# Optimization experiments

Hardware: AMD Instinct MI355X
Metric: run time of the kernel (lower is better)

Reference implementation:

```python
import jax, jax.numpy as jnp
import numpy as np

N = 10000      # nodes per graph
E = 160000     # random edges per graph (plus N self-loops)
IN_DIM = 4096
HID = 64       # num_hidden
H = 8          # heads
C = 5          # num_classes
SLOPE = 0.2    # LeakyReLU negative slope


def gat_conv(x, src, dst, W, al, ar, b, res_W=None):
    """DGL-style GATConv. x:(N,F) -> (N,H,D). Messages flow src->dst,
    edge softmax over in-edges of each dst node."""
    n = x.shape[0]
    h, d = al.shape
    feat = (x @ W).reshape(n, h, d)                      # (N,H,D)
    el = jnp.sum(feat * al, axis=-1)                     # (N,H)
    er = jnp.sum(feat * ar, axis=-1)                     # (N,H)
    e = jax.nn.leaky_relu(el[src] + er[dst], SLOPE)      # (E,H)
    emax = jax.ops.segment_max(e, dst, num_segments=n)   # (N,H) stable softmax
    ex = jnp.exp(e - emax[dst])
    denom = jax.ops.segment_sum(ex, dst, num_segments=n)
    alpha = ex / denom[dst]                              # (E,H)
    out = jax.ops.segment_sum(feat[src] * alpha[..., None], dst, num_segments=n)
    if res_W is not None:
        out = out + (x @ res_W).reshape(n, h, d)         # residual projection
    return out + b.reshape(h, d)


def encoder(x, src, dst, W0, al0, ar0, b0, W1, al1, ar1, b1):
    h0 = jax.nn.elu(gat_conv(x, src, dst, W0, al0, ar0, b0))   # (N,H,D)
    h0 = h0.reshape(h0.shape[0], -1)                           # flatten(1)
    return jax.nn.elu(gat_conv(h0, src, dst, W1, al1, ar1, b1))


def setup_inputs() -> dict:
    key = jax.random.key(0)
    ks = list(jax.random.split(key, 40))
    ki = iter(ks)

    def edges(k):
        k1, k2 = jax.random.split(k)
        loop = jnp.arange(N, dtype=jnp.int32)
        s = jnp.concatenate([jax.random.randint(k1, (E,), 0, N, dtype=jnp.int32), loop])
        d = jnp.concatenate([jax.random.randint(k2, (E,), 0, N, dtype=jnp.int32), loop])
        return s, d

    inp = {}
    for name in ("s0", "s1", "t"):
        s, d = edges(next(ki))
        inp[f"src_{name}"], inp[f"dst_{name}"] = s, d
    inp["features_s0"] = jax.random.normal(next(ki), (N, IN_DIM), jnp.float32)
    inp["features_s1"] = jax.random.normal(next(ki), (N, IN_DIM), jnp.float32)
    inp["features_t"]  = jax.random.normal(next(ki), (N, IN_DIM), jnp.float32)

    def lin(k, fan_in, fan_out):
        return jax.random.normal(k, (fan_in, fan_out), jnp.float32) / np.sqrt(fan_in)

    inp["W0"] = lin(next(ki), IN_DIM, H * HID)
    inp["al0"] = 0.1 * jax.random.normal(next(ki), (H, HID), jnp.float32)
    inp["ar0"] = 0.1 * jax.random.normal(next(ki), (H, HID), jnp.float32)
    inp["b0"] = jnp.zeros((H * HID,), jnp.float32)
    inp["W1"] = lin(next(ki), H * HID, H * HID)
    inp["al1"] = 0.1 * jax.random.normal(next(ki), (H, HID), jnp.float32)
    inp["ar1"] = 0.1 * jax.random.normal(next(ki), (H, HID), jnp.float32)
    inp["b1"] = jnp.zeros((H * HID,), jnp.float32)
    for k_idx in (0, 1):
        inp[f"Wc{k_idx}"] = lin(next(ki), H * HID, H * C)
        inp[f"alc{k_idx}"] = 0.1 * jax.random.normal(next(ki), (H, C), jnp.float32)
        inp[f"arc{k_idx}"] = 0.1 * jax.random.normal(next(ki), (H, C), jnp.float32)
        inp[f"bc{k_idx}"] = jnp.zeros((H * C,), jnp.float32)
        inp[f"rW{k_idx}"] = lin(next(ki), H * HID, H * C)
    inp["num_source"] = 2
    return inp


def reference(features_s0, features_s1, features_t,
              W0, al0, ar0, b0, W1, al1, ar1, b1,
              Wc0, alc0, arc0, bc0, rW0,
              Wc1, alc1, arc1, bc1, rW1,
              src_s0, dst_s0, src_s1, dst_s1, src_t, dst_t,
              num_source):
    enc_p = (W0, al0, ar0, b0, W1, al1, ar1, b1)
    cls_p = [(Wc0, alc0, arc0, bc0, rW0), (Wc1, alc1, arc1, bc1, rW1)]
    feats = [features_s0, features_s1]
    graphs = [(src_s0, dst_s0), (src_s1, dst_s1)]

    # shared-weight encoder on each source graph
    h_s = [encoder(feats[i], graphs[i][0], graphs[i][1], *enc_p)
           for i in range(num_source)]                    # each (N,H,HID)
    # per-source classifiers on their own graphs, mean over heads
    pred_s = []
    for i in range(num_source):
        Wc, alc, arc, bc, rW = cls_p[i]
        s, d = graphs[i]
        logits = gat_conv(h_s[i].reshape(N, -1), s, d, Wc, alc, arc, bc, res_W=rW)
        pred_s.append(logits.mean(axis=1))               # (N,C)
    emb_s = [h.reshape(N, -1) for h in h_s]

    # target: every source classifier applied to the target graph
    h_t = encoder(features_t, src_t, dst_t, *enc_p)
    pred_t = []
    for i in range(num_source):
        Wc, alc, arc, bc, rW = cls_p[i]
        logits = gat_conv(h_t.reshape(N, -1), src_t, dst_t, Wc, alc, arc, bc, res_W=rW)
        pred_t.append(logits.mean(axis=1))
    emb_t = h_t.reshape(N, -1)

    return (pred_s[0], pred_s[1], pred_t[0], pred_t[1], emb_s[0], emb_s[1], emb_t)
```

## Files before the change

### kernel.cpp

```cpp
#include <hip/hip_runtime.h>
#include <stdint.h>

typedef _Float16 f16;
typedef _Float16 f16x2 __attribute__((ext_vector_type(2)));
typedef _Float16 f16x8 __attribute__((ext_vector_type(8)));
typedef float f32x4 __attribute__((ext_vector_type(4)));

#define AS1 __attribute__((address_space(1)))
#define AS3 __attribute__((address_space(3)))

#define NN 10000
#define NP 10112
#define KK0 4096
#define FF 512

__global__ void k_count_b(const int* __restrict__ d0, const int* __restrict__ d1,
                          const int* __restrict__ d2, int E0, int E1, int E2,
                          int nb0, int nb1, int* __restrict__ deg){
  int b = blockIdx.x;
  const int* d; int Eg, base, lb;
  if (b < nb0){ d=d0; Eg=E0; base=0; lb=b; }
  else if (b < nb0+nb1){ d=d1; Eg=E1; base=NN; lb=b-nb0; }
  else { d=d2; Eg=E2; base=2*NN; lb=b-nb0-nb1; }
  int i = lb*256 + threadIdx.x;
  if (i < Eg) atomicAdd(&deg[base + d[i]], 1);
}

__global__ __launch_bounds__(1024) void k_scan_b(const int* __restrict__ deg_all,
    int* __restrict__ rowptr_all, int* __restrict__ cursor_all){
  int g = blockIdx.x;
  const int* deg = deg_all + g*NN;
  int* rowptr = rowptr_all + g*(NN+1);
  int* cursor = cursor_all + g*NN;
  __shared__ int ps[1024];
  int t = threadIdx.x;
  const int CH = 16;
  int i0 = t*CH;
  int sum = 0;
  for (int k=0;k<CH;k++){ int i=i0+k; if (i<NN) sum += deg[i]; }
  ps[t]=sum; __syncthreads();
  for (int off=1; off<1024; off<<=1){
    int v = (t>=off)? ps[t-off] : 0;
    __syncthreads();
    ps[t] += v;
    __syncthreads();
  }
  int run = ps[t]-sum;
  for (int k=0;k<CH;k++){
    int i=i0+k;
    if (i<=NN) rowptr[i]=run;
    if (i<NN){ cursor[i]=run; run += deg[i]; }
  }
}

__global__ void k_fill_b(const int* __restrict__ s0, const int* __restrict__ d0,
                         const int* __restrict__ s1, const int* __restrict__ d1,
                         const int* __restrict__ s2, const int* __restrict__ d2,
                         int E0, int E1, int E2, int nb0, int nb1,
                         int* __restrict__ cursor_all,
                         int* __restrict__ c0, int* __restrict__ c1, int* __restrict__ c2){
  int b = blockIdx.x;
  const int *s, *d; int Eg, lb; int* cur; int* col;
  if (b < nb0){ s=s0; d=d0; Eg=E0; lb=b; cur=cursor_all; col=c0; }
  else if (b < nb0+nb1){ s=s1; d=d1; Eg=E1; lb=b-nb0; cur=cursor_all+NN; col=c1; }
  else { s=s2; d=d2; Eg=E2; lb=b-nb0-nb1; cur=cursor_all+2*NN; col=c2; }
  int i = lb*256 + threadIdx.x;
  if (i >= Eg) return;
  int slot = atomicAdd(&cur[d[i]], 1);
  col[slot] = s[i];
}

__global__ void k_transpose_t(const float* __restrict__ W, f16* __restrict__ WT,
                              int K, int Nc){
  __shared__ float tile[32][33];
  int n0 = blockIdx.x*32, k0 = blockIdx.y*32;
  int tx = threadIdx.x, ty = threadIdx.y;
  #pragma unroll
  for (int i=0;i<32;i+=8)
    tile[ty+i][tx] = W[(long)(k0+ty+i)*Nc + n0+tx];
  __syncthreads();
  #pragma unroll
  for (int i=0;i<32;i+=8)
    WT[(long)(n0+ty+i)*K + k0+tx] = (f16)tile[tx][ty+i];
}

__global__ void k_pack_wc(const float* __restrict__ Wc, const float* __restrict__ rW,
                          f16* __restrict__ WT){
  int idx = blockIdx.x*256 + threadIdx.x;
  if (idx >= 128*512) return;
  int n = idx >> 9; int k = idx & 511;
  float v = 0.f;
  if (n < 40) v = Wc[k*40 + n];
  else if (n < 80) v = rW[k*40 + (n-40)];
  WT[idx] = (f16)v;
}

__global__ __launch_bounds__(256,3) void k_gemm0(
    const float* __restrict__ X0, const float* __restrict__ X1, const float* __restrict__ X2,
    f16* __restrict__ C0, f16* __restrict__ C1, f16* __restrict__ C2,
    const f16* __restrict__ B,
    const float* __restrict__ alp, const float* __restrict__ arp,
    float* __restrict__ elp, float* __restrict__ erp)
{
  __shared__ f16 lds[2][12288];
  const int bid = blockIdx.x;
  const int task = bid / 632;
  const int orig = bid - task*632;
  const int wid = (orig & 7)*79 + (orig >> 3);
  const int tr = wid >> 2, tc = wid & 3;
  const float* A = task==0 ? X0 : (task==1 ? X1 : X2);
  f16* C = task==0 ? C0 : (task==1 ? C1 : C2);

  const int t = threadIdx.x;
  const int wave = t >> 6, lane = t & 63;
  const int wr = wave >> 1, wc = wave & 1;

  const f16* Bb = B + (long)tc*128*KK0;
  const int slot = (lane&7) ^ (lane>>3);
  const int rbase = wave*8 + (lane>>3);

  const int arow0 = t >> 3;
  const int ak8 = t & 7;
  const float* gA[2];
  bool okA[2];
  #pragma unroll
  for (int s=0;s<2;s++){
    int grow = tr*64 + arow0 + s*32;
    okA[s] = grow < NN;
    gA[s] = A + (long)(okA[s] ? grow : 0)*KK0 + ak8*8;
  }
  f32x4 arE[2][2];

  #define LOADA(kt) { \
    _Pragma("unroll") \
    for (int s=0;s<2;s++){ \
      arE[s][0] = *(const f32x4*)(gA[s] + (kt)*64); \
      arE[s][1] = *(const f32x4*)(gA[s] + (kt)*64 + 4); \
    } }

  #define WRITEA(buf) { \
    _Pragma("unroll") \
    for (int s=0;s<2;s++){ \
      int row = arow0 + s*32; \
      f16x8 v; \
      _Pragma("unroll") \
      for (int j=0;j<4;j++){ \
        v[j]   = okA[s] ? (f16)arE[s][0][j] : (f16)0.f; \
        v[4+j] = okA[s] ? (f16)arE[s][1][j] : (f16)0.f; \
      } \
      *(f16x8*)(&lds[buf][row*64 + ((ak8 ^ (row&7))*8)]) = v; \
    } }

  #define GLDSB(kt, buf) { \
    int ko = (kt)*64; \
    _Pragma("unroll") \
    for (int i=0;i<4;i++) \
      __builtin_amdgcn_global_load_lds((const AS1 void*)(Bb + ko + (i*32+rbase)*KK0 + slot*8), \
          (AS3 void*)(&lds[buf][4096 + i*2048 + wave*512]), 16, 0, 0); \
    }

  f32x4 zero4 = {0.f,0.f,0.f,0.f};
  f32x4 acc[2][4];
  #pragma unroll
  for (int m=0;m<2;m++)
    #pragma unroll
    for (int n=0;n<4;n++) acc[m][n] = zero4;

  int abyte[2][2], bbyte[2][4];
  #pragma unroll
  for (int ks=0;ks<2;ks++){
    #pragma unroll
    for (int m=0;m<2;m++){
      int row = wr*32 + m*16 + (lane&15);
      abyte[ks][m] = row*128 + (((ks*4 + (lane>>4))*16) ^ ((row&7)<<4));
    }
    #pragma unroll
    for (int n=0;n<4;n++){
      int brow = wc*64 + n*16 + (lane&15);
      bbyte[ks][n] = 8192 + brow*128 + (((ks*4 + (lane>>4))*16) ^ ((brow&7)<<4));
    }
  }

  const int nt = KK0 >> 6;

  LOADA(0);
  __builtin_amdgcn_sched_barrier(0);
  GLDSB(0, 0);
  __builtin_amdgcn_sched_barrier(0);
  WRITEA(0);
  __builtin_amdgcn_sched_barrier(0);
  LOADA(1);
  __builtin_amdgcn_sched_barrier(0);
  asm volatile("s_waitcnt vmcnt(4) lgkmcnt(0)" ::: "memory");
  __builtin_amdgcn_s_barrier();

  int cur = 0;
  for (int kt=0; kt<nt; kt++){
    if (kt+1 < nt){
      WRITEA(cur^1);
      __builtin_amdgcn_sched_barrier(0);
      GLDSB(kt+1, cur^1);
      __builtin_amdgcn_sched_barrier(0);
    }
    if (kt+2 < nt){
      LOADA(kt+2);
      __builtin_amdgcn_sched_barrier(0);
    }
    const char* Ls = (const char*)&lds[cur][0];
    #pragma unroll
    for (int ks=0;ks<2;ks++){
      f16x8 af[2], bf[4];
      #pragma unroll
      for (int m=0;m<2;m++) af[m] = *(const f16x8*)(Ls + abyte[ks][m]);
      #pragma unroll
      for (int n=0;n<4;n++) bf[n] = *(const f16x8*)(Ls + bbyte[ks][n]);
      #pragma unroll
      for (int m=0;m<2;m++)
        #pragma unroll
        for (int n=0;n<4;n++)
          acc[m][n] = __builtin_amdgcn_mfma_f32_16x16x32_f16(af[m], bf[n], acc[m][n], 0, 0, 0);
    }
    if (kt+1 < nt){
      __builtin_amdgcn_sched_barrier(0);
      if (kt+2 < nt)
        asm volatile("s_waitcnt vmcnt(4) lgkmcnt(0)" ::: "memory");
      else
        asm volatile("s_waitcnt vmcnt(0) lgkmcnt(0)" ::: "memory");
      __builtin_amdgcn_s_barrier();
    }
    cur ^= 1;
  }
  #undef LOADA
  #undef WRITEA
  #undef GLDSB

  #pragma unroll
  for (int m=0;m<2;m++){
    int row0 = tr*64 + wr*32 + m*16 + ((lane>>4)<<2);
    #pragma unroll
    for (int n=0;n<4;n++){
      int col = tc*128 + wc*64 + n*16 + (lane&15);
      #pragma unroll
      for (int q2=0;q2<4;q2++)
        C[(long)(row0+q2)*FF + col] = (f16)acc[m][n][q2];
    }
  }

  {
    int head = tc*2 + wc;
    const float* alh = alp + head*64;
    const float* arh = arp + head*64;
    float alv[4], arv[4];
    #pragma unroll
    for (int n=0;n<4;n++){ int d = n*16 + (lane&15); alv[n]=alh[d]; arv[n]=arh[d]; }
    float* elo = elp + (long)task*NN*8;
    float* ero = erp + (long)task*NN*8;
    #pragma unroll
    for (int m=0;m<2;m++){
      float e0,e1,e2,e3,r0,r1,r2,r3;
      #pragma unroll
      for (int q=0;q<4;q++){
        float e=0.f, r=0.f;
        #pragma unroll
        for (int n=0;n<4;n++){ e += acc[m][n][q]*alv[n]; r += acc[m][n][q]*arv[n]; }
        #pragma unroll
        for (int off=1; off<16; off<<=1){ e += __shfl_xor(e, off); r += __shfl_xor(r, off); }
        if (q==0){e0=e;r0=r;} else if (q==1){e1=e;r1=r;} else if (q==2){e2=e;r2=r;} else {e3=e;r3=r;}
      }
      int q = lane&15;
      if (q < 4){
        int node = tr*64 + wr*32 + m*16 + ((lane>>4)<<2) + q;
        if (node < NN){
          float ev = q==0?e0:(q==1?e1:(q==2?e2:e3));
          float rv = q==0?r0:(q==1?r1:(q==2?r2:r3));
          long o = (long)node*8 + head;
          elo[o] = ev;
          ero[o] = rv;
        }
      }
    }
  }
}

struct GemmTasks { const f16* A[4]; const f16* B[4]; f16* C[4]; };

__global__ __launch_bounds__(256,3) void k_gemmb(GemmTasks p, int ntpb, int ntn,
                                                 int Nc, int K,
                                                 const float* __restrict__ alp,
                                                 const float* __restrict__ arp,
                                                 float* __restrict__ elp,
                                                 float* __restrict__ erp){
  __shared__ f16 lds[2][12288];
  const int bid = blockIdx.x;
  const int task = bid / ntpb;
  const int orig = bid - task*ntpb;
  const int q = ntpb >> 3, r = ntpb & 7;
  const int xcd = orig & 7, bx = orig >> 3;
  const int wid = (xcd < r ? xcd*(q+1) : r*(q+1) + (xcd-r)*q) + bx;
  const int tr = wid / ntn, tc = wid - tr*ntn;

  const f16* A = p.A[task];
  const f16* B = p.B[task];
  f16* C = p.C[task];

  const int t = threadIdx.x;
  const int wave = t >> 6, lane = t & 63;
  const int wr = wave >> 1, wc = wave & 1;

  const f16* Ab = A + (long)tr*64*K;
  const f16* Bb = B + (long)tc*128*K;

  const int slot = (lane&7) ^ (lane>>3);
  const int rbase = wave*8 + (lane>>3);

  f32x4 zero4 = {0.f,0.f,0.f,0.f};
  f32x4 acc[2][4];
  #pragma unroll
  for (int m=0;m<2;m++)
    #pragma unroll
    for (int n=0;n<4;n++) acc[m][n] = zero4;

  int abyte[2][2], bbyte[2][4];
  #pragma unroll
  for (int ks=0;ks<2;ks++){
    #pragma unroll
    for (int m=0;m<2;m++){
      int row = wr*32 + m*16 + (lane&15);
      abyte[ks][m] = row*128 + (((ks*4 + (lane>>4))*16) ^ ((row&7)<<4));
    }
    #pragma unroll
    for (int n=0;n<4;n++){
      int brow = wc*64 + n*16 + (lane&15);
      bbyte[ks][n] = 8192 + brow*128 + (((ks*4 + (lane>>4))*16) ^ ((brow&7)<<4));
    }
  }

  const int nt = K >> 6;
  int cur = 0;

  #pragma unroll
  for (int i=0;i<2;i++)
    __builtin_amdgcn_global_load_lds((const AS1 void*)(Ab + (i*32+rbase)*K + slot*8),
        (AS3 void*)(&lds[0][i*2048 + wave*512]), 16, 0, 0);
  #pragma unroll
  for (int i=0;i<4;i++)
    __builtin_amdgcn_global_load_lds((const AS1 void*)(Bb + (i*32+rbase)*K + slot*8),
        (AS3 void*)(&lds[0][4096 + i*2048 + wave*512]), 16, 0, 0);
  __syncthreads();

  for (int kt=0; kt<nt; kt++){
    if (kt+1 < nt){
      int ko = (kt+1)<<6;
      #pragma unroll
      for (int i=0;i<2;i++)
        __builtin_amdgcn_global_load_lds((const AS1 void*)(Ab + ko + (i*32+rbase)*K + slot*8),
            (AS3 void*)(&lds[cur^1][i*2048 + wave*512]), 16, 0, 0);
      #pragma unroll
      for (int i=0;i<4;i++)
        __builtin_amdgcn_global_load_lds((const AS1 void*)(Bb + ko + (i*32+rbase)*K + slot*8),
            (AS3 void*)(&lds[cur^1][4096 + i*2048 + wave*512]), 16, 0, 0);
    }
    const char* Ls = (const char*)&lds[cur][0];
    #pragma unroll
    for (int ks=0;ks<2;ks++){
      f16x8 af[2], bf[4];
      #pragma unroll
      for (int m=0;m<2;m++) af[m] = *(const f16x8*)(Ls + abyte[ks][m]);
      #pragma unroll
      for (int n=0;n<4;n++) bf[n] = *(const f16x8*)(Ls + bbyte[ks][n]);
      #pragma unroll
      for (int m=0;m<2;m++)
        #pragma unroll
        for (int n=0;n<4;n++)
          acc[m][n] = __builtin_amdgcn_mfma_f32_16x16x32_f16(af[m], bf[n], acc[m][n], 0, 0, 0);
    }
    __syncthreads();
    cur ^= 1;
  }

  #pragma unroll
  for (int m=0;m<2;m++){
    int row0 = tr*64 + wr*32 + m*16 + ((lane>>4)<<2);
    #pragma unroll
    for (int n=0;n<4;n++){
      int col = tc*128 + wc*64 + n*16 + (lane&15);
      #pragma unroll
      for (int q2=0;q2<4;q2++)
        C[(long)(row0+q2)*Nc + col] = (f16)acc[m][n][q2];
    }
  }

  if (alp){
    int head = tc*2 + wc;
    const float* alh = alp + head*64;
    const float* arh = arp + head*64;
    float alv[4], arv[4];
    #pragma unroll
    for (int n=0;n<4;n++){ int d = n*16 + (lane&15); alv[n]=alh[d]; arv[n]=arh[d]; }
    float* elo = elp + (long)task*NN*8;
    float* ero = erp + (long)task*NN*8;
    #pragma unroll
    for (int m=0;m<2;m++){
      float e0,e1,e2,e3,r0,r1,r2,r3;
      #pragma unroll
      for (int qq=0;qq<4;qq++){
        float e=0.f, rr=0.f;
        #pragma unroll
        for (int n=0;n<4;n++){ e += acc[m][n][qq]*alv[n]; rr += acc[m][n][qq]*arv[n]; }
        #pragma unroll
        for (int off=1; off<16; off<<=1){ e += __shfl_xor(e, off); rr += __shfl_xor(rr, off); }
        if (qq==0){e0=e;r0=rr;} else if (qq==1){e1=e;r1=rr;} else if (qq==2){e2=e;r2=rr;} else {e3=e;r3=rr;}
      }
      int qq = lane&15;
      if (qq < 4){
        int node = tr*64 + wr*32 + m*16 + ((lane>>4)<<2) + qq;
        if (node < NN){
          float ev = qq==0?e0:(qq==1?e1:(qq==2?e2:e3));
          float rv = qq==0?r0:(qq==1?r1:(qq==2?r2:r3));
          long o = (long)node*8 + head;
          elo[o] = ev;
          ero[o] = rv;
        }
      }
    }
  }
}

#define MAXD 128

struct AggArgs {
  const int* rp[3]; const int* cs[3];
  const float* el; const float* er;
  const f16* feat[3];
  const float* bias;
  f16* outH[3];
  float* outF[3];
};

__global__ __launch_bounds__(256) void k_agg_b(AggArgs a){
  int b = blockIdx.x;
  int g = b / NN, n = b - g*NN;
  const int* rowptr = a.rp[g];
  const int* colsrc = a.cs[g];
  const float* el = a.el + (long)g*NN*8;
  const f16* featH = a.feat[g];
  int t = threadIdx.x;
  __shared__ float sm[MAXD*8];
  __shared__ int   scol[MAXD];
  __shared__ float red[256];
  __shared__ float inv[8];
  __shared__ float ern[8];
  if (t < 8) ern[t] = a.er[((long)g*NN+n)*8+t];
  __syncthreads();
  int j0 = rowptr[n], deg = rowptr[n+1]-j0;
  {
    int h = t & 7;
    float dsum = 0.f;
    for (int jj = t>>3; jj < deg; jj += 32){
      int s = colsrc[j0+jj];
      float v = el[s*8+h] + ern[h];
      v = (v>0.f)? v : 0.2f*v;
      float ex = __expf(v);
      dsum += ex;
      if (jj < MAXD){
        sm[jj*8+h] = ex;
        if (h==0) scol[jj] = s;
      }
    }
    red[t] = dsum; __syncthreads();
    if (t<128) red[t] += red[t+128]; __syncthreads();
    if (t<64)  red[t] += red[t+64];  __syncthreads();
    if (t<32)  red[t] += red[t+32];  __syncthreads();
    if (t<16)  red[t] += red[t+16];  __syncthreads();
    if (t<8)   inv[t] = 1.0f / (red[t] + red[t+8]);
    __syncthreads();
  }
  int h = t >> 5;
  int c = t*2;
  float a0=0.f, a1=0.f;
  float ivh = inv[h];
  for (int jj=0; jj<deg; jj++){
    int s; float ex;
    if (jj < MAXD){ s = scol[jj]; ex = sm[jj*8+h]; }
    else {
      s = colsrc[j0+jj];
      float v = el[s*8+h] + ern[h];
      v = (v>0.f)? v : 0.2f*v;
      ex = __expf(v);
    }
    float alpha = ex * ivh;
    f16x2 f = *(const f16x2*)(featH + (long)s*FF + c);
    a0 += alpha*(float)f[0];
    a1 += alpha*(float)f[1];
  }
  a0 += a.bias[c]; a1 += a.bias[c+1];
  a0 = (a0>0.f)? a0 : __expf(a0)-1.f;
  a1 = (a1>0.f)? a1 : __expf(a1)-1.f;
  f16x2 o; o[0]=(f16)a0; o[1]=(f16)a1;
  *(f16x2*)(a.outH[g] + (long)n*FF + c) = o;
  float* oF = a.outF[g];
  if (oF){
    oF[(long)n*FF + c]     = a0;
    oF[(long)n*FF + c + 1] = a1;
  }
}

__global__ void k_elerc_b(const f16* __restrict__ fc,
    const float* __restrict__ alc0, const float* __restrict__ arc0,
    const float* __restrict__ alc1, const float* __restrict__ arc1,
    float* __restrict__ el, float* __restrict__ er){
  int idx = blockIdx.x*256 + threadIdx.x;
  if (idx >= 4*NN*8) return;
  int ti = idx / (NN*8);
  int rem = idx - ti*NN*8;
  int n = rem>>3, hh = rem&7;
  const f16* featc = fc + (long)ti*NP*128;
  const float* al = (ti&1) ? alc1 : alc0;
  const float* ar_ = (ti&1) ? arc1 : arc0;
  float a=0.f, bsum=0.f;
  #pragma unroll
  for (int cc=0; cc<5; cc++){
    float v = (float)featc[(long)n*128 + hh*5 + cc];
    a += v*al[hh*5+cc];
    bsum += v*ar_[hh*5+cc];
  }
  el[idx]=a; er[idx]=bsum;
}

struct ClsArgs {
  const int* rp[3]; const int* cs[3];
  const float* el; const float* er;
  const f16* fc;
  const float* bc[2];
  float* pred;
};

__global__ __launch_bounds__(64) void k_cls_b(ClsArgs a){
  int b = blockIdx.x;
  int ti = b / NN, n = b - ti*NN;
  int g = ti<2 ? ti : 2;
  int ci = ti&1;
  const int* rowptr = a.rp[g];
  const int* colsrc = a.cs[g];
  const float* el = a.el + (long)ti*NN*8;
  const f16* featc = a.fc + (long)ti*NP*128;
  const float* bc = a.bc[ci];
  float* pred = a.pred + (long)ti*5*NN;
  int l = threadIdx.x;
  __shared__ float sm[MAXD*8];
  __shared__ int   scol[MAXD];
  __shared__ float inv[8];
  __shared__ float ern[8];
  __shared__ float lg[40];
  if (l<8) ern[l] = a.er[((long)ti*NN+n)*8+l];
  __syncthreads();
  int j0 = rowptr[n], deg = rowptr[n+1]-j0;
  {
    int h = l & 7;
    float dsum = 0.f;
    for (int jj = l>>3; jj < deg; jj += 8){
      int s = colsrc[j0+jj];
      float v = el[s*8+h] + ern[h];
      v = (v>0.f)? v : 0.2f*v;
      float ex = __expf(v);
      dsum += ex;
      if (jj < MAXD){
        sm[jj*8+h] = ex;
        if (h==0) scol[jj] = s;
      }
    }
    dsum += __shfl_xor(dsum, 8);
    dsum += __shfl_xor(dsum, 16);
    dsum += __shfl_xor(dsum, 32);
    if (l<8) inv[l] = 1.0f/dsum;
  }
  __syncthreads();
  if (l<40){
    int h = l/5;
    float ivh = inv[h];
    float acc = 0.f;
    for (int jj=0; jj<deg; jj++){
      int s; float ex;
      if (jj < MAXD){ s = scol[jj]; ex = sm[jj*8+h]; }
      else {
        s = colsrc[j0+jj];
        float v = el[s*8+h] + ern[h];
        v = (v>0.f)? v : 0.2f*v;
        ex = __expf(v);
      }
      acc += ex*ivh * (float)featc[(long)s*128 + l];
    }
    acc += (float)featc[(long)n*128 + 40 + l];
    acc += bc[l];
    lg[l] = acc;
  }
  __syncthreads();
  if (l<5){
    float p=0.f;
    #pragma unroll
    for (int h=0;h<8;h++) p += lg[h*5+l];
    pred[(long)n*5 + l] = p*0.125f;
  }
}

extern "C" void kernel_launch(void* const* d_in, const int* in_sizes, int n_in,
                              void* d_out, int out_size, void* d_ws, size_t ws_size,
                              hipStream_t stream){
  const int* srcs[3] = {(const int*)d_in[0], (const int*)d_in[2], (const int*)d_in[4]};
  const int* dsts[3] = {(const int*)d_in[1], (const int*)d_in[3], (const int*)d_in[5]};
  int E[3] = {in_sizes[0], in_sizes[2], in_sizes[4]};
  const float* X[3] = {(const float*)d_in[6], (const float*)d_in[7], (const float*)d_in[8]};
  const float* W0  = (const float*)d_in[9];
  const float* al0 = (const float*)d_in[10];
  const float* ar0 = (const float*)d_in[11];
  const float* b0  = (const float*)d_in[12];
  const float* W1  = (const float*)d_in[13];
  const float* al1 = (const float*)d_in[14];
  const float* ar1 = (const float*)d_in[15];
  const float* b1  = (const float*)d_in[16];
  const float* Wcv[2] = {(const float*)d_in[17], (const float*)d_in[22]};
  const float* alc[2] = {(const float*)d_in[18], (const float*)d_in[23]};
  const float* arc[2] = {(const float*)d_in[19], (const float*)d_in[24]};
  const float* bcv[2] = {(const float*)d_in[20], (const float*)d_in[25]};
  const float* rWv[2] = {(const float*)d_in[21], (const float*)d_in[26]};

  float* out = (float*)d_out;
  float* embOut[3] = {out+200000, out+200000+(long)NN*FF, out+200000+2L*NN*FF};

  char* w = (char*)d_ws;
  size_t off = 0;
  auto alloc = [&](size_t bytes)->void*{
    void* p = (void*)(w + off);
    off += (bytes + 255) & ~((size_t)255);
    return p;
  };
  f16* W0T = (f16*)alloc((size_t)FF*KK0*2);
  f16* W1T = (f16*)alloc((size_t)FF*FF*2);
  f16* WcT[2] = {(f16*)alloc(128*512*2), (f16*)alloc(128*512*2)};
  f16* feat0H[3], *h0H[3], *feat1H[3], *embH[3];
  for (int g=0;g<3;g++) feat0H[g] = (f16*)alloc((size_t)NP*FF*2);
  for (int g=0;g<3;g++) h0H[g]    = (f16*)alloc((size_t)NP*FF*2);
  for (int g=0;g<3;g++) feat1H[g] = (f16*)alloc((size_t)NP*FF*2);
  for (int g=0;g<3;g++) embH[g]   = (f16*)alloc((size_t)NP*FF*2);
  f16* featc = (f16*)alloc((size_t)4*NP*128*2);
  float* el_e = (float*)alloc((size_t)3*NN*8*4);
  float* er_e = (float*)alloc((size_t)3*NN*8*4);
  float* el_c = (float*)alloc((size_t)4*NN*8*4);
  float* er_c = (float*)alloc((size_t)4*NN*8*4);
  int* deg    = (int*)alloc((size_t)3*NN*4);
  int* cursor = (int*)alloc((size_t)3*NN*4);
  int* rowptr = (int*)alloc((size_t)3*(NN+1)*4);
  int* colsrc[3];
  for (int g=0;g<3;g++) colsrc[g] = (int*)alloc((size_t)E[g]*4);
  (void)ws_size; (void)n_in; (void)out_size;

  int nb[3] = {(E[0]+255)/256, (E[1]+255)/256, (E[2]+255)/256};
  hipMemsetAsync(deg, 0, (size_t)3*NN*4, stream);
  k_count_b<<<nb[0]+nb[1]+nb[2], 256, 0, stream>>>(dsts[0], dsts[1], dsts[2],
      E[0], E[1], E[2], nb[0], nb[1], deg);
  k_scan_b<<<3, 1024, 0, stream>>>(deg, rowptr, cursor);
  k_fill_b<<<nb[0]+nb[1]+nb[2], 256, 0, stream>>>(srcs[0], dsts[0], srcs[1], dsts[1],
      srcs[2], dsts[2], E[0], E[1], E[2], nb[0], nb[1], cursor,
      colsrc[0], colsrc[1], colsrc[2]);

  k_transpose_t<<<dim3(FF/32, KK0/32), dim3(32,8), 0, stream>>>(W0, W0T, KK0, FF);
  k_transpose_t<<<dim3(FF/32, FF/32), dim3(32,8), 0, stream>>>(W1, W1T, FF, FF);
  k_pack_wc<<<(128*512+255)/256, 256, 0, stream>>>(Wcv[0], rWv[0], WcT[0]);
  k_pack_wc<<<(128*512+255)/256, 256, 0, stream>>>(Wcv[1], rWv[1], WcT[1]);

  const int* rp[3] = {rowptr, rowptr+(NN+1), rowptr+2*(NN+1)};

  k_gemm0<<<3*632, 256, 0, stream>>>(X[0], X[1], X[2],
      feat0H[0], feat0H[1], feat0H[2], W0T, al0, ar0, el_e, er_e);
  {
    AggArgs a;
    for (int g=0;g<3;g++){ a.rp[g]=rp[g]; a.cs[g]=colsrc[g]; a.feat[g]=feat0H[g];
                           a.outH[g]=h0H[g]; a.outF[g]=nullptr; }
    a.el = el_e; a.er = er_e; a.bias = b0;
    k_agg_b<<<3*NN, 256, 0, stream>>>(a);
  }

  {
    GemmTasks p;
    for (int i=0;i<4;i++){ int g = i<3?i:0; p.A[i]=h0H[g]; p.B[i]=W1T; p.C[i]=feat1H[g]; }
    k_gemmb<<<3*632, 256, 0, stream>>>(p, 632, 4, FF, FF, al1, ar1, el_e, er_e);
  }
  {
    AggArgs a;
    for (int g=0;g<3;g++){ a.rp[g]=rp[g]; a.cs[g]=colsrc[g]; a.feat[g]=feat1H[g];
                           a.outH[g]=embH[g]; a.outF[g]=embOut[g]; }
    a.el = el_e; a.er = er_e; a.bias = b1;
    k_agg_b<<<3*NN, 256, 0, stream>>>(a);
  }

  {
    GemmTasks p;
    const int tg[4] = {0,1,2,2};
    for (int i=0;i<4;i++){ p.A[i]=embH[tg[i]]; p.B[i]=WcT[i&1]; p.C[i]=featc + (long)i*NP*128; }
    k_gemmb<<<4*158, 256, 0, stream>>>(p, 158, 1, 128, FF,
        (const float*)nullptr, (const float*)nullptr, (float*)nullptr, (float*)nullptr);
  }
  k_elerc_b<<<(4*NN*8+255)/256, 256, 0, stream>>>(featc, alc[0], arc[0], alc[1], arc[1], el_c, er_c);
  {
    ClsArgs a;
    for (int g=0;g<3;g++){ a.rp[g]=rp[g]; a.cs[g]=colsrc[g]; }
    a.el = el_c; a.er = er_c; a.fc = featc;
    a.bc[0] = bcv[0]; a.bc[1] = bcv[1];
    a.pred = out;
    k_cls_b<<<4*NN, 64, 0, stream>>>(a);
  }
}
```

Measured before the change: 617.1 us.

## Use wide 64x512 GEMM tiles so each block reads its A rows once

The two feature GEMMs (layer 0 with fp32->fp16 conversion, layer 1 in fp16) are replaced by one templated kernel. Each 512-thread block computes a full 64x512 output row strip, one wave per head, instead of four separate 64x128 tiles. Each A row is now loaded and converted once rather than four times, and the el/er head reductions stay inside one block. The cost is a 144KB double-buffered LDS footprint allowing one block per CU, and only 474 blocks, which lowers occupancy and latency hiding.

New measurement: 615.4 us. About the same (-0.3%).

```diff
diff --git a/kernel.cpp b/kernel.cpp
--- a/kernel.cpp
+++ b/kernel.cpp
@@ -95,151 +95,165 @@
   WT[idx] = (f16)v;
 }
 
-__global__ __launch_bounds__(256,3) void k_gemm0(
-    const float* __restrict__ X0, const float* __restrict__ X1, const float* __restrict__ X2,
+template<bool CVT>
+__global__ __launch_bounds__(512,1) void k_gemmw(
+    const void* __restrict__ A0v, const void* __restrict__ A1v, const void* __restrict__ A2v,
     f16* __restrict__ C0, f16* __restrict__ C1, f16* __restrict__ C2,
     const f16* __restrict__ B,
     const float* __restrict__ alp, const float* __restrict__ arp,
     float* __restrict__ elp, float* __restrict__ erp)
 {
-  __shared__ f16 lds[2][12288];
-  const int bid = blockIdx.x;
-  const int task = bid / 632;
-  const int orig = bid - task*632;
-  const int wid = (orig & 7)*79 + (orig >> 3);
-  const int tr = wid >> 2, tc = wid & 3;
-  const float* A = task==0 ? X0 : (task==1 ? X1 : X2);
-  f16* C = task==0 ? C0 : (task==1 ? C1 : C2);
+  constexpr int K = CVT ? KK0 : FF;
+  constexpr int nt = K >> 6;
+  __shared__ f16 lds[2][36864];
+
+  const int nwg = gridDim.x;
+  const int qd = nwg>>3, rd = nwg&7;
+  const int xcd = blockIdx.x & 7, bx = blockIdx.x >> 3;
+  const int wid = (xcd < rd ? xcd*(qd+1) : rd*(qd+1) + (xcd-rd)*qd) + bx;
+  const int task = wid / 158;
+  const int tr = wid - task*158;
+
+  f16* C = task==0?C0:(task==1?C1:C2);
 
   const int t = threadIdx.x;
   const int wave = t >> 6, lane = t & 63;
-  const int wr = wave >> 1, wc = wave & 1;
-
-  const f16* Bb = B + (long)tc*128*KK0;
   const int slot = (lane&7) ^ (lane>>3);
-  const int rbase = wave*8 + (lane>>3);
-
-  const int arow0 = t >> 3;
+  const int arow = t >> 3;
   const int ak8 = t & 7;
-  const float* gA[2];
-  bool okA[2];
-  #pragma unroll
-  for (int s=0;s<2;s++){
-    int grow = tr*64 + arow0 + s*32;
-    okA[s] = grow < NN;
-    gA[s] = A + (long)(okA[s] ? grow : 0)*KK0 + ak8*8;
-  }
-  f32x4 arE[2][2];
-
-  #define LOADA(kt) { \
+
+  #define GLDSB(kt, buf) { \
+    int ko = (kt)*64; \
     _Pragma("unroll") \
-    for (int s=0;s<2;s++){ \
-      arE[s][0] = *(const f32x4*)(gA[s] + (kt)*64); \
-      arE[s][1] = *(const f32x4*)(gA[s] + (kt)*64 + 4); \
+    for (int i=0;i<8;i++){ \
+      int br = i*64 + wave*8 + (lane>>3); \
+      __builtin_amdgcn_global_load_lds((const AS1 void*)(B + (long)br*K + ko + slot*8), \
+          (AS3 void*)(&lds[buf][4096 + i*4096 + wave*512]), 16, 0, 0); \
     } }
 
-  #define WRITEA(buf) { \
+  int abyte[2][4], bbyte[2][4];
+  #pragma unroll
+  for (int ks=0;ks<2;ks++){
+    #pragma unroll
+    for (int m=0;m<4;m++){
+      int row = m*16 + (lane&15);
+      abyte[ks][m] = row*128 + (((ks*4 + (lane>>4))*16) ^ ((row&7)<<4));
+    }
+    #pragma unroll
+    for (int n=0;n<4;n++){
+      int brow = wave*64 + n*16 + (lane&15);
+      bbyte[ks][n] = 8192 + brow*128 + (((ks*4 + (lane>>4))*16) ^ ((brow&7)<<4));
+    }
+  }
+
+  f32x4 zero4 = {0.f,0.f,0.f,0.f};
+  f32x4 acc[4][4];
+  #pragma unroll
+  for (int m=0;m<4;m++)
+    #pragma unroll
+    for (int n=0;n<4;n++) acc[m][n] = zero4;
+
+  #define MFMA_TILE(buf) { \
+    const char* Ls = (const char*)&lds[buf][0]; \
     _Pragma("unroll") \
-    for (int s=0;s<2;s++){ \
-      int row = arow0 + s*32; \
+    for (int ks=0;ks<2;ks++){ \
+      f16x8 af[4], bf[4]; \
+      _Pragma("unroll") \
+      for (int m=0;m<4;m++) af[m] = *(const f16x8*)(Ls + abyte[ks][m]); \
+      _Pragma("unroll") \
+      for (int n=0;n<4;n++) bf[n] = *(const f16x8*)(Ls + bbyte[ks][n]); \
+      _Pragma("unroll") \
+      for (int m=0;m<4;m++) \
+        _Pragma("unroll") \
+        for (int n=0;n<4;n++) \
+          acc[m][n] = __builtin_amdgcn_mfma_f32_16x16x32_f16(af[m], bf[n], acc[m][n], 0, 0, 0); \
+    } }
+
+  int cur = 0;
+  if constexpr (CVT){
+    const float* Af = task==0?(const float*)A0v:(task==1?(const float*)A1v:(const float*)A2v);
+    const bool okA = (tr*64 + arow) < NN;
+    const float* gA = Af + (long)(okA ? tr*64+arow : 0)*KK0 + ak8*8;
+    f32x4 arE0, arE1;
+
+    #define LOADA(kt) { arE0 = *(const f32x4*)(gA + (kt)*64); \
+                        arE1 = *(const f32x4*)(gA + (kt)*64 + 4); }
+    #define WRITEA(buf) { \
       f16x8 v; \
       _Pragma("unroll") \
       for (int j=0;j<4;j++){ \
-        v[j]   = okA[s] ? (f16)arE[s][0][j] : (f16)0.f; \
-        v[4+j] = okA[s] ? (f16)arE[s][1][j] : (f16)0.f; \
+        v[j]   = okA ? (f16)arE0[j] : (f16)0.f; \
+        v[4+j] = okA ? (f16)arE1[j] : (f16)0.f; \
       } \
-      *(f16x8*)(&lds[buf][row*64 + ((ak8 ^ (row&7))*8)]) = v; \
-    } }
-
-  #define GLDSB(kt, buf) { \
-    int ko = (kt)*64; \
-    _Pragma("unroll") \
-    for (int i=0;i<4;i++) \
-      __builtin_amdgcn_global_load_lds((const AS1 void*)(Bb + ko + (i*32+rbase)*KK0 + slot*8), \
-          (AS3 void*)(&lds[buf][4096 + i*2048 + wave*512]), 16, 0, 0); \
-    }
-
-  f32x4 zero4 = {0.f,0.f,0.f,0.f};
-  f32x4 acc[2][4];
-  #pragma unroll
-  for (int m=0;m<2;m++)
-    #pragma unroll
-    for (int n=0;n<4;n++) acc[m][n] = zero4;
-
-  int abyte[2][2], bbyte[2][4];
-  #pragma unroll
-  for (int ks=0;ks<2;ks++){
-    #pragma unroll
-    for (int m=0;m<2;m++){
-      int row = wr*32 + m*16 + (lane&15);
-      abyte[ks][m] = row*128 + (((ks*4 + (lane>>4))*16) ^ ((row&7)<<4));
-    }
+      *(f16x8*)(&lds[buf][arow*64 + ((ak8 ^ (arow&7))*8)]) = v; }
+
+    LOADA(0);
+    __builtin_amdgcn_sched_barrier(0);
+    GLDSB(0, 0);
+    __builtin_amdgcn_sched_barrier(0);
+    WRITEA(0);
+    __builtin_amdgcn_sched_barrier(0);
+    LOADA(1);
+    __builtin_amdgcn_sched_barrier(0);
+    asm volatile("s_waitcnt vmcnt(2) lgkmcnt(0)" ::: "memory");
+    __builtin_amdgcn_s_barrier();
+
+    for (int kt=0; kt<nt; kt++){
+      if (kt+1 < nt){
+        WRITEA(cur^1);
+        __builtin_amdgcn_sched_barrier(0);
+        GLDSB(kt+1, cur^1);
+        __builtin_amdgcn_sched_barrier(0);
+      }
+      if (kt+2 < nt){
+        LOADA(kt+2);
+        __builtin_amdgcn_sched_barrier(0);
+      }
+      MFMA_TILE(cur);
+      if (kt+1 < nt){
+        __builtin_amdgcn_sched_barrier(0);
+        if (kt+2 < nt)
+          asm volatile("s_waitcnt vmcnt(2) lgkmcnt(0)" ::: "memory");
+        else
+          asm volatile("s_waitcnt vmcnt(0) lgkmcnt(0)" ::: "memory");
+        __builtin_amdgcn_s_barrier();
+      }
+      cur ^= 1;
+    }
+    #undef LOADA
+    #undef WRITEA
+  } else {
+    const f16* Ah = task==0?(const f16*)A0v:(task==1?(const f16*)A1v:(const f16*)A2v);
+    const f16* Ab = Ah + (long)tr*64*K;
+    const int aslot = ak8 ^ (arow&7);
+
+    #define GLDSA(kt, buf) \
+      __builtin_amdgcn_global_load_lds((const AS1 void*)(Ab + (long)arow*K + (kt)*64 + aslot*8), \
+          (AS3 void*)(&lds[buf][wave*512]), 16, 0, 0);
+
+    GLDSA(0, 0);
+    GLDSB(0, 0);
+    __syncthreads();
+    for (int kt=0; kt<nt; kt++){
+      if (kt+1 < nt){
+        GLDSA(kt+1, cur^1);
+        GLDSB(kt+1, cur^1);
+      }
+      MFMA_TILE(cur);
+      __syncthreads();
+      cur ^= 1;
+    }
+    #undef GLDSA
+  }
+  #undef GLDSB
+  #undef MFMA_TILE
+
+  #pragma unroll
+  for (int m=0;m<4;m++){
+    int row0 = tr*64 + m*16 + ((lane>>4)<<2);
     #pragma unroll
     for (int n=0;n<4;n++){
-      int brow = wc*64 + n*16 + (lane&15);
-      bbyte[ks][n] = 8192 + brow*128 + (((ks*4 + (lane>>4))*16) ^ ((brow&7)<<4));
-    }
-  }
-
-  const int nt = KK0 >> 6;
-
-  LOADA(0);
-  __builtin_amdgcn_sched_barrier(0);
-  GLDSB(0, 0);
-  __builtin_amdgcn_sched_barrier(0);
-  WRITEA(0);
-  __builtin_amdgcn_sched_barrier(0);
-  LOADA(1);
-  __builtin_amdgcn_sched_barrier(0);
-  asm volatile("s_waitcnt vmcnt(4) lgkmcnt(0)" ::: "memory");
-  __builtin_amdgcn_s_barrier();
-
-  int cur = 0;
-  for (int kt=0; kt<nt; kt++){
-    if (kt+1 < nt){
-      WRITEA(cur^1);
-      __builtin_amdgcn_sched_barrier(0);
-      GLDSB(kt+1, cur^1);
-      __builtin_amdgcn_sched_barrier(0);
-    }
-    if (kt+2 < nt){
-      LOADA(kt+2);
-      __builtin_amdgcn_sched_barrier(0);
-    }
-    const char* Ls = (const char*)&lds[cur][0];
-    #pragma unroll
-    for (int ks=0;ks<2;ks++){
-      f16x8 af[2], bf[4];
-      #pragma unroll
-      for (int m=0;m<2;m++) af[m] = *(const f16x8*)(Ls + abyte[ks][m]);
-      #pragma unroll
-      for (int n=0;n<4;n++) bf[n] = *(const f16x8*)(Ls + bbyte[ks][n]);
-      #pragma unroll
-      for (int m=0;m<2;m++)
-        #pragma unroll
-        for (int n=0;n<4;n++)
-          acc[m][n] = __builtin_amdgcn_mfma_f32_16x16x32_f16(af[m], bf[n], acc[m][n], 0, 0, 0);
-    }
-    if (kt+1 < nt){
-      __builtin_amdgcn_sched_barrier(0);
-      if (kt+2 < nt)
-        asm volatile("s_waitcnt vmcnt(4) lgkmcnt(0)" ::: "memory");
-      else
-        asm volatile("s_waitcnt vmcnt(0) lgkmcnt(0)" ::: "memory");
-      __builtin_amdgcn_s_barrier();
-    }
-    cur ^= 1;
-  }
-  #undef LOADA
-  #undef WRITEA
-  #undef GLDSB
-
-  #pragma unroll
-  for (int m=0;m<2;m++){
-    int row0 = tr*64 + wr*32 + m*16 + ((lane>>4)<<2);
-    #pragma unroll
-    for (int n=0;n<4;n++){
-      int col = tc*128 + wc*64 + n*16 + (lane&15);
+      int col = wave*64 + n*16 + (lane&15);
       #pragma unroll
       for (int q2=0;q2<4;q2++)
         C[(long)(row0+q2)*FF + col] = (f16)acc[m][n][q2];
@@ -247,7 +261,7 @@
   }
 
   {
-    int head = tc*2 + wc;
+    const int head = wave;
     const float* alh = alp + head*64;
     const float* arh = arp + head*64;
     float alv[4], arv[4];
@@ -256,23 +270,23 @@
     float* elo = elp + (long)task*NN*8;
     float* ero = erp + (long)task*NN*8;
     #pragma unroll
-    for (int m=0;m<2;m++){
+    for (int m=0;m<4;m++){
       float e0,e1,e2,e3,r0,r1,r2,r3;
       #pragma unroll
-      for (int q=0;q<4;q++){
-        float e=0.f, r=0.f;
+      for (int qq=0;qq<4;qq++){
+        float e=0.f, rr=0.f;
         #pragma unroll
-        for (int n=0;n<4;n++){ e += acc[m][n][q]*alv[n]; r += acc[m][n][q]*arv[n]; }
+        for (int n=0;n<4;n++){ e += acc[m][n][qq]*alv[n]; rr += acc[m][n][qq]*arv[n]; }
         #pragma unroll
-        for (int off=1; off<16; off<<=1){ e += __shfl_xor(e, off); r += __shfl_xor(r, off); }
-        if (q==0){e0=e;r0=r;} else if (q==1){e1=e;r1=r;} else if (q==2){e2=e;r2=r;} else {e3=e;r3=r;}
-      }
-      int q = lane&15;
-      if (q < 4){
-        int node = tr*64 + wr*32 + m*16 + ((lane>>4)<<2) + q;
+        for (int off=1; off<16; off<<=1){ e += __shfl_xor(e, off); rr += __shfl_xor(rr, off); }
+        if (qq==0){e0=e;r0=rr;} else if (qq==1){e1=e;r1=rr;} else if (qq==2){e2=e;r2=rr;} else {e3=e;r3=rr;}
+      }
+      int qq = lane&15;
+      if (qq < 4){
+        int node = tr*64 + m*16 + ((lane>>4)<<2) + qq;
         if (node < NN){
-          float ev = q==0?e0:(q==1?e1:(q==2?e2:e3));
-          float rv = q==0?r0:(q==1?r1:(q==2?r2:r3));
+          float ev = qq==0?e0:(qq==1?e1:(qq==2?e2:e3));
+          float rv = qq==0?r0:(qq==1?r1:(qq==2?r2:r3));
           long o = (long)node*8 + head;
           elo[o] = ev;
           ero[o] = rv;
@@ -285,11 +299,7 @@
 struct GemmTasks { const f16* A[4]; const f16* B[4]; f16* C[4]; };
 
 __global__ __launch_bounds__(256,3) void k_gemmb(GemmTasks p, int ntpb, int ntn,
-                                                 int Nc, int K,
-                                                 const float* __restrict__ alp,
-                                                 const float* __restrict__ arp,
-                                                 float* __restrict__ elp,
-                                                 float* __restrict__ erp){
+                                                 int Nc, int K){
   __shared__ f16 lds[2][12288];
   const int bid = blockIdx.x;
   const int task = bid / ntpb;
@@ -387,41 +397,6 @@
       #pragma unroll
       for (int q2=0;q2<4;q2++)
         C[(long)(row0+q2)*Nc + col] = (f16)acc[m][n][q2];
-    }
-  }
-
-  if (alp){
-    int head = tc*2 + wc;
-    const float* alh = alp + head*64;
-    const float* arh = arp + head*64;
-    float alv[4], arv[4];
-    #pragma unroll
-    for (int n=0;n<4;n++){ int d = n*16 + (lane&15); alv[n]=alh[d]; arv[n]=arh[d]; }
-    float* elo = elp + (long)task*NN*8;
-    float* ero = erp + (long)task*NN*8;
-    #pragma unroll
-    for (int m=0;m<2;m++){
-      float e0,e1,e2,e3,r0,r1,r2,r3;
-      #pragma unroll
-      for (int qq=0;qq<4;qq++){
-        float e=0.f, rr=0.f;
-        #pragma unroll
-        for (int n=0;n<4;n++){ e += acc[m][n][qq]*alv[n]; rr += acc[m][n][qq]*arv[n]; }
-        #pragma unroll
-        for (int off=1; off<16; off<<=1){ e += __shfl_xor(e, off); rr += __shfl_xor(rr, off); }
-        if (qq==0){e0=e;r0=rr;} else if (qq==1){e1=e;r1=rr;} else if (qq==2){e2=e;r2=rr;} else {e3=e;r3=rr;}
-      }
-      int qq = lane&15;
-      if (qq < 4){
-        int node = tr*64 + wr*32 + m*16 + ((lane>>4)<<2) + qq;
-        if (node < NN){
-          float ev = qq==0?e0:(qq==1?e1:(qq==2?e2:e3));
-          float rv = qq==0?r0:(qq==1?r1:(qq==2?r2:r3));
-          long o = (long)node*8 + head;
-          elo[o] = ev;
-          ero[o] = rv;
-        }
-      }
     }
   }
 }
@@ -670,7 +645,7 @@
 
   const int* rp[3] = {rowptr, rowptr+(NN+1), rowptr+2*(NN+1)};
 
-  k_gemm0<<<3*632, 256, 0, stream>>>(X[0], X[1], X[2],
+  k_gemmw<true><<<474, 512, 0, stream>>>(X[0], X[1], X[2],
       feat0H[0], feat0H[1], feat0H[2], W0T, al0, ar0, el_e, er_e);
   {
     AggArgs a;
@@ -680,11 +655,8 @@
     k_agg_b<<<3*NN, 256, 0, stream>>>(a);
   }
 
-  {
-    GemmTasks p;
-    for (int i=0;i<4;i++){ int g = i<3?i:0; p.A[i]=h0H[g]; p.B[i]=W1T; p.C[i]=feat1H[g]; }
-    k_gemmb<<<3*632, 256, 0, stream>>>(p, 632, 4, FF, FF, al1, ar1, el_e, er_e);
-  }
+  k_gemmw<false><<<474, 512, 0, stream>>>(h0H[0], h0H[1], h0H[2],
+      feat1H[0], feat1H[1], feat1H[2], W1T, al1, ar1, el_e, er_e);
   {
     AggArgs a;
     for (int g=0;g<3;g++){ a.rp[g]=rp[g]; a.cs[g]=colsrc[g]; a.feat[g]=feat1H[g];
@@ -697,8 +669,7 @@
     GemmTasks p;
     const int tg[4] = {0,1,2,2};
     for (int i=0;i<4;i++){ p.A[i]=embH[tg[i]]; p.B[i]=WcT[i&1]; p.C[i]=featc + (long)i*NP*128; }
-    k_gemmb<<<4*158, 256, 0, stream>>>(p, 158, 1, 128, FF,
-        (const float*)nullptr, (const float*)nullptr, (float*)nullptr, (float*)nullptr);
+    k_gemmb<<<4*158, 256, 0, stream>>>(p, 158, 1, 128, FF);
   }
   k_elerc_b<<<(4*NN*8+255)/256, 256, 0, stream>>>(featc, alc[0], arc[0], alc[1], arc[1], el_c, er_c);
   {
```
